# Kernel tuning notes

Hardware: AMD Instinct MI355X
Metric: run time of the kernel (lower is better)

The kernel has to match this reference:

```python
import jax, jax.numpy as jnp
import numpy as np

N, E = 50000, 800000
IN, HID, L, HEADS, OUT = 128, 256, 8, 8, 40
DH = HID // HEADS


def setup_inputs() -> dict:
    key = jax.random.key(0)
    ks = jax.random.split(key, 12)
    s = 0.05
    d = {}
    d["X"] = jax.random.normal(ks[0], (N, IN), jnp.float32)
    d["src"] = jax.random.randint(ks[1], (E,), 0, N, dtype=jnp.int32)
    d["dst"] = jax.random.randint(ks[2], (E,), 0, N, dtype=jnp.int32)
    d["Win"] = jax.random.normal(ks[3], (IN, HID), jnp.float32) * s
    d["bin_"] = jnp.zeros((HID,), jnp.float32)
    d["Wq"] = jax.random.normal(ks[4], (L, HID, HID), jnp.float32) * s
    d["Wk"] = jax.random.normal(ks[5], (L, HID, HID), jnp.float32) * s
    d["Wv"] = jax.random.normal(ks[6], (L, HID, HID), jnp.float32) * s
    d["bq"] = jnp.zeros((L, HID), jnp.float32)
    d["bk"] = jnp.zeros((L, HID), jnp.float32)
    d["bv"] = jnp.zeros((L, HID), jnp.float32)
    d["Wout"] = jax.random.normal(ks[7], (HID, OUT), jnp.float32) * s
    d["bout"] = jnp.zeros((OUT,), jnp.float32)
    return d


def _segment_softmax(e, seg, n):
    # e: [E, H] edge scores, seg: [E] destination node ids
    m = jax.ops.segment_max(e, seg, num_segments=n)
    ex = jnp.exp(e - m[seg])
    s = jax.ops.segment_sum(ex, seg, num_segments=n)
    return ex / s[seg]


def reference(X, src, dst, Win, bin_, Wq, Wk, Wv, bq, bk, bv, Wout, bout):
    n = X.shape[0]
    scaling = DH ** -0.5
    h = X @ Win + bin_  # in_proj: [N, HID]
    for l in range(L):  # fixed small layer stack
        q = (h @ Wq[l] + bq[l]).reshape(n, HEADS, DH) * scaling
        k = (h @ Wk[l] + bk[l]).reshape(n, HEADS, DH)
        v = (h @ Wv[l] + bv[l]).reshape(n, HEADS, DH)
        # SDDMM: per-edge, per-head dot product q[dst] . k[src]
        e = jnp.einsum('ehd,ehd->eh', q[dst], k[src])  # [E, HEADS]
        a = _segment_softmax(e, dst, n)                # softmax over in-edges of each dst
        # SpMM: weighted aggregation of source values into destinations
        h = jax.ops.segment_sum(a[..., None] * v[src], dst, num_segments=n).reshape(n, HID)
    return h @ Wout + bout  # predictor: [N, OUT]
```

## Files before the change

kernel.cpp:

```cpp
#include <hip/hip_runtime.h>
#include <hip/hip_bf16.h>
#include <hip/hip_fp16.h>

#define N_NODES 50000
#define MPAD    50048
#define N_EDGES 800000
#define IN_DIM  128
#define HID     256
#define QKVW    768
#define N_LAYERS 8
#define OUT_DIM 40
#define SCALING 0.17677669529663687f

typedef __attribute__((ext_vector_type(8))) _Float16 f16x8;
typedef __attribute__((ext_vector_type(4))) float f32x4;

__device__ __forceinline__ void gload_lds16(const void* g, void* l) {
    __builtin_amdgcn_global_load_lds(
        (__attribute__((address_space(1))) const unsigned int*)g,
        (__attribute__((address_space(3))) unsigned int*)l, 16, 0, 0);
}

__global__ void hist_kernel(const int* __restrict__ dst, int* __restrict__ cnt, int E) {
    int e = blockIdx.x * blockDim.x + threadIdx.x;
    if (e < E) atomicAdd(&cnt[dst[e]], 1);
}

__global__ __launch_bounds__(1024) void scan_kernel(const int* __restrict__ cnt,
                                                    int* __restrict__ row_off, int n) {
    __shared__ int buf[1024];
    __shared__ int carry_s;
    int tid = threadIdx.x;
    if (tid == 0) carry_s = 0;
    __syncthreads();
    for (int base = 0; base < n; base += 1024) {
        int i = base + tid;
        int x = (i < n) ? cnt[i] : 0;
        buf[tid] = x;
        __syncthreads();
        for (int off = 1; off < 1024; off <<= 1) {
            int y = (tid >= off) ? buf[tid - off] : 0;
            __syncthreads();
            buf[tid] += y;
            __syncthreads();
        }
        int carry = carry_s;
        if (i < n) row_off[i] = carry + buf[tid] - x;
        int total = buf[1023];
        __syncthreads();
        if (tid == 0) carry_s = carry + total;
        __syncthreads();
    }
    if (tid == 0) row_off[n] = carry_s;
}

__global__ void scatter_kernel(const int* __restrict__ src, const int* __restrict__ dst,
                               const int* __restrict__ row_off, int* __restrict__ cur,
                               int* __restrict__ csr_src, int E) {
    int e = blockIdx.x * blockDim.x + threadIdx.x;
    if (e < E) {
        int d = dst[e];
        int pos = row_off[d] + atomicAdd(&cur[d], 1);
        csr_src[pos] = src[e];
    }
}

__global__ void wqkv_cvt_kernel(const float* __restrict__ Wq, const float* __restrict__ Wk,
                                const float* __restrict__ Wv, _Float16* __restrict__ outw) {
    int i = blockIdx.x * blockDim.x + threadIdx.x;
    if (i >= N_LAYERS * QKVW * HID) return;
    int k = i & 255;
    int n = (i >> 8) % QKVW;
    int l = i / (QKVW * HID);
    int seg = n >> 8, nn = n & 255;
    const float* W = (seg == 0) ? Wq : (seg == 1) ? Wk : Wv;
    outw[i] = (_Float16)W[((size_t)l * HID + k) * HID + nn];
}

__global__ void win_cvt_kernel(const float* __restrict__ Win, _Float16* __restrict__ outw) {
    int i = blockIdx.x * blockDim.x + threadIdx.x;
    if (i >= HID * IN_DIM) return;
    int k = i & 127;
    int n = i >> 7;
    outw[i] = (_Float16)Win[(size_t)k * HID + n];
}

__global__ void wout_cvt_kernel(const float* __restrict__ Wout, _Float16* __restrict__ hi,
                                _Float16* __restrict__ lo) {
    int i = blockIdx.x * blockDim.x + threadIdx.x;
    if (i >= 128 * HID) return;
    int k = i & 255;
    int n = i >> 8;
    float v = (n < OUT_DIM) ? Wout[(size_t)k * OUT_DIM + n] : 0.f;
    _Float16 h = (_Float16)v;
    hi[i] = h;
    lo[i] = (_Float16)(v - (float)h);
}

__global__ void x_cvt_kernel(const float* __restrict__ X, _Float16* __restrict__ outx) {
    int i = blockIdx.x * blockDim.x + threadIdx.x;
    if (i >= MPAD * IN_DIM) return;
    int r = i >> 7;
    outx[i] = (_Float16)((r < N_NODES) ? X[i] : 0.f);
}

__global__ __launch_bounds__(256) void gemm16(
        const _Float16* __restrict__ A, const _Float16* __restrict__ B,
        const float* __restrict__ bias0, const float* __restrict__ bias1,
        const float* __restrict__ bias2, float scale0,
        _Float16* __restrict__ C, int K, int ldC) {
    __shared__ __align__(16) _Float16 lds[2 * 4096];
    _Float16* ldsA = lds;
    _Float16* ldsB = lds + 4096;

    const int tid  = threadIdx.x;
    const int lane = tid & 63;
    const int wave = tid >> 6;
    const int row0 = blockIdx.y * 128;
    const int n0   = blockIdx.x * 128;

    const int p0 = wave * 64 + lane;
    const int p1 = p0 + 256;
    auto srcoff = [&](int p, int grow0) -> size_t {
        int row = p >> 2, cir = p & 3;
        int sw  = (row & 3) ^ ((row >> 2) & 3);
        int sc  = cir ^ sw;
        return (size_t)(grow0 + row) * K + sc * 8;
    };
    const size_t offA0 = srcoff(p0, row0), offA1 = srcoff(p1, row0);
    const size_t offB0 = srcoff(p0, n0),   offB1 = srcoff(p1, n0);
    const int d0 = wave * 512;
    const int d1 = 2048 + wave * 512;

    const int mh = (wave >> 1) * 64;
    const int nh = (wave & 1) * 64;
    int aoff[4], boff[4];
#pragma unroll
    for (int f = 0; f < 4; ++f) {
        int ra = mh + f * 16 + (lane & 15);
        int ca = (lane >> 4) ^ ((ra & 3) ^ ((ra >> 2) & 3));
        aoff[f] = ra * 64 + ca * 16;
        int rb = nh + f * 16 + (lane & 15);
        int cb = (lane >> 4) ^ ((rb & 3) ^ ((rb >> 2) & 3));
        boff[f] = rb * 64 + cb * 16;
    }

    f32x4 acc[4][4];
#pragma unroll
    for (int i = 0; i < 4; ++i)
#pragma unroll
        for (int j = 0; j < 4; ++j) acc[i][j] = {0.f, 0.f, 0.f, 0.f};

    for (int k0 = 0; k0 < K; k0 += 32) {
        gload_lds16(A + offA0 + k0, ldsA + d0);
        gload_lds16(A + offA1 + k0, ldsA + d1);
        gload_lds16(B + offB0 + k0, ldsB + d0);
        gload_lds16(B + offB1 + k0, ldsB + d1);
        __syncthreads();
        f16x8 af[4];
#pragma unroll
        for (int i = 0; i < 4; ++i)
            af[i] = *reinterpret_cast<const f16x8*>(reinterpret_cast<const char*>(ldsA) + aoff[i]);
#pragma unroll
        for (int j = 0; j < 4; ++j) {
            f16x8 bf = *reinterpret_cast<const f16x8*>(reinterpret_cast<const char*>(ldsB) + boff[j]);
#pragma unroll
            for (int i = 0; i < 4; ++i)
                acc[i][j] = __builtin_amdgcn_mfma_f32_16x16x32_f16(af[i], bf, acc[i][j], 0, 0, 0);
        }
        __syncthreads();
    }

    const int seg = n0 >> 8;
    const float* bias = (seg == 0) ? bias0 : (seg == 1) ? bias1 : bias2;
    const float scale = (seg == 0) ? scale0 : 1.f;
    const int fq = lane >> 4;
    const int fr = lane & 15;
#pragma unroll
    for (int i = 0; i < 4; ++i) {
#pragma unroll
        for (int j = 0; j < 4; ++j) {
#pragma unroll
            for (int r = 0; r < 4; ++r) {
                int m = row0 + mh + i * 16 + fq * 4 + r;
                int n = n0 + nh + j * 16 + fr;
                float o = (acc[i][j][r] + bias[n & 255]) * scale;
                C[(size_t)m * ldC + n] = (_Float16)o;
            }
        }
    }
}

__global__ __launch_bounds__(256) void gemm_out(
        const _Float16* __restrict__ A, const _Float16* __restrict__ Bh,
        const _Float16* __restrict__ Bl, const float* __restrict__ bias,
        float* __restrict__ C, int K) {
    __shared__ __align__(16) _Float16 lds[3 * 4096];
    _Float16* ldsA  = lds;
    _Float16* ldsBh = lds + 4096;
    _Float16* ldsBl = lds + 8192;

    const int tid  = threadIdx.x;
    const int lane = tid & 63;
    const int wave = tid >> 6;
    const int row0 = blockIdx.y * 128;

    const int p0 = wave * 64 + lane;
    const int p1 = p0 + 256;
    auto srcoff = [&](int p, int grow0) -> size_t {
        int row = p >> 2, cir = p & 3;
        int sw  = (row & 3) ^ ((row >> 2) & 3);
        int sc  = cir ^ sw;
        return (size_t)(grow0 + row) * K + sc * 8;
    };
    const size_t offA0 = srcoff(p0, row0), offA1 = srcoff(p1, row0);
    const size_t offB0 = srcoff(p0, 0),    offB1 = srcoff(p1, 0);
    const int d0 = wave * 512;
    const int d1 = 2048 + wave * 512;

    const int mh = (wave >> 1) * 64;
    const int nh = (wave & 1) * 64;
    int aoff[4], boff[4];
#pragma unroll
    for (int f = 0; f < 4; ++f) {
        int ra = mh + f * 16 + (lane & 15);
        int ca = (lane >> 4) ^ ((ra & 3) ^ ((ra >> 2) & 3));
        aoff[f] = ra * 64 + ca * 16;
        int rb = nh + f * 16 + (lane & 15);
        int cb = (lane >> 4) ^ ((rb & 3) ^ ((rb >> 2) & 3));
        boff[f] = rb * 64 + cb * 16;
    }

    f32x4 acc[4][4];
#pragma unroll
    for (int i = 0; i < 4; ++i)
#pragma unroll
        for (int j = 0; j < 4; ++j) acc[i][j] = {0.f, 0.f, 0.f, 0.f};

    for (int k0 = 0; k0 < K; k0 += 32) {
        gload_lds16(A + offA0 + k0, ldsA + d0);
        gload_lds16(A + offA1 + k0, ldsA + d1);
        gload_lds16(Bh + offB0 + k0, ldsBh + d0);
        gload_lds16(Bh + offB1 + k0, ldsBh + d1);
        gload_lds16(Bl + offB0 + k0, ldsBl + d0);
        gload_lds16(Bl + offB1 + k0, ldsBl + d1);
        __syncthreads();
        f16x8 af[4];
#pragma unroll
        for (int i = 0; i < 4; ++i)
            af[i] = *reinterpret_cast<const f16x8*>(reinterpret_cast<const char*>(ldsA) + aoff[i]);
#pragma unroll
        for (int j = 0; j < 4; ++j) {
            f16x8 bh = *reinterpret_cast<const f16x8*>(reinterpret_cast<const char*>(ldsBh) + boff[j]);
            f16x8 bl = *reinterpret_cast<const f16x8*>(reinterpret_cast<const char*>(ldsBl) + boff[j]);
#pragma unroll
            for (int i = 0; i < 4; ++i) {
                acc[i][j] = __builtin_amdgcn_mfma_f32_16x16x32_f16(af[i], bh, acc[i][j], 0, 0, 0);
                acc[i][j] = __builtin_amdgcn_mfma_f32_16x16x32_f16(af[i], bl, acc[i][j], 0, 0, 0);
            }
        }
        __syncthreads();
    }

    const int fq = lane >> 4;
    const int fr = lane & 15;
#pragma unroll
    for (int i = 0; i < 4; ++i) {
#pragma unroll
        for (int j = 0; j < 4; ++j) {
#pragma unroll
            for (int r = 0; r < 4; ++r) {
                int m = row0 + mh + i * 16 + fq * 4 + r;
                int n = nh + j * 16 + fr;
                if (m < N_NODES && n < OUT_DIM)
                    C[(size_t)m * OUT_DIM + n] = acc[i][j][r] + bias[n];
            }
        }
    }
}

__global__ __launch_bounds__(256) void attn_kernel(
        const _Float16* __restrict__ qkv, const int* __restrict__ row_off,
        const int* __restrict__ csr_src, _Float16* __restrict__ h_out, int n) {
    int wave = threadIdx.x >> 6;
    int lane = threadIdx.x & 63;
    int node = blockIdx.x * 4 + wave;
    if (node >= n) return;
    const int loff = lane * 4;
    float4 qv;
    {
        float2 raw = *reinterpret_cast<const float2*>(&qkv[(size_t)node * QKVW + loff]);
        const __half2* h2 = reinterpret_cast<const __half2*>(&raw);
        float2 a = __half22float2(h2[0]), b = __half22float2(h2[1]);
        qv = make_float4(a.x, a.y, b.x, b.y);
    }
    float4 acc = make_float4(0.f, 0.f, 0.f, 0.f);
    float m = -INFINITY, s = 0.f;
    int beg = row_off[node], end = row_off[node + 1];
    int idx = beg;

#define LOAD_KV(slot, sn)                                                                 \
    float2 kr##slot, vr##slot;                                                            \
    {                                                                                     \
        const _Float16* base = qkv + (size_t)(sn) * QKVW;                                 \
        kr##slot = *reinterpret_cast<const float2*>(base + HID + loff);                   \
        vr##slot = *reinterpret_cast<const float2*>(base + 2 * HID + loff);               \
    }

#define DOT(slot, dvar)                                                                   \
    float dvar;                                                                           \
    {                                                                                     \
        const __half2* kh = reinterpret_cast<const __half2*>(&kr##slot);                  \
        float2 k01 = __half22float2(kh[0]), k23 = __half22float2(kh[1]);                  \
        dvar = qv.x * k01.x + qv.y * k01.y + qv.z * k23.x + qv.w * k23.y;                 \
        dvar += __shfl_xor(dvar, 1);                                                      \
        dvar += __shfl_xor(dvar, 2);                                                      \
        dvar += __shfl_xor(dvar, 4);                                                      \
    }

#define VADD(slot, p)                                                                     \
    {                                                                                     \
        const __half2* vh = reinterpret_cast<const __half2*>(&vr##slot);                  \
        float2 v01 = __half22float2(vh[0]), v23 = __half22float2(vh[1]);                  \
        acc.x = fmaf(p, v01.x, acc.x);                                                    \
        acc.y = fmaf(p, v01.y, acc.y);                                                    \
        acc.z = fmaf(p, v23.x, acc.z);                                                    \
        acc.w = fmaf(p, v23.y, acc.w);                                                    \
    }

    for (; idx + 3 < end; idx += 4) {
        int s0 = csr_src[idx], s1 = csr_src[idx + 1];
        int s2 = csr_src[idx + 2], s3 = csr_src[idx + 3];
        LOAD_KV(0, s0) LOAD_KV(1, s1) LOAD_KV(2, s2) LOAD_KV(3, s3)
        DOT(0, e0) DOT(1, e1) DOT(2, e2) DOT(3, e3)
        float mn = fmaxf(fmaxf(fmaxf(m, e0), fmaxf(e1, e2)), e3);
        float c  = __expf(m - mn);
        float p0 = __expf(e0 - mn), p1 = __expf(e1 - mn);
        float p2 = __expf(e2 - mn), p3 = __expf(e3 - mn);
        s = fmaf(s, c, (p0 + p1) + (p2 + p3));
        acc.x *= c; acc.y *= c; acc.z *= c; acc.w *= c;
        VADD(0, p0) VADD(1, p1) VADD(2, p2) VADD(3, p3)
        m = mn;
    }
    for (; idx < end; ++idx) {
        int s0 = csr_src[idx];
        LOAD_KV(0, s0)
        DOT(0, e0)
        float mn = fmaxf(m, e0);
        float c = __expf(m - mn);
        float p0 = __expf(e0 - mn);
        s = fmaf(s, c, p0);
        acc.x *= c; acc.y *= c; acc.z *= c; acc.w *= c;
        VADD(0, p0)
        m = mn;
    }
#undef LOAD_KV
#undef DOT
#undef VADD

    float inv = (s > 0.f) ? 1.f / s : 0.f;
    __half2 o01 = __floats2half2_rn(acc.x * inv, acc.y * inv);
    __half2 o23 = __floats2half2_rn(acc.z * inv, acc.w * inv);
    union { __half2 h2[2]; float2 f2; } u;
    u.h2[0] = o01; u.h2[1] = o23;
    *reinterpret_cast<float2*>(&h_out[(size_t)node * HID + loff]) = u.f2;
}

extern "C" void kernel_launch(void* const* d_in, const int* in_sizes, int n_in,
                              void* d_out, int out_size, void* d_ws, size_t ws_size,
                              hipStream_t stream) {
    const float* X    = (const float*)d_in[0];
    const int*   src  = (const int*)d_in[1];
    const int*   dst  = (const int*)d_in[2];
    const float* Win  = (const float*)d_in[3];
    const float* bin_ = (const float*)d_in[4];
    const float* Wq   = (const float*)d_in[5];
    const float* Wk   = (const float*)d_in[6];
    const float* Wv   = (const float*)d_in[7];
    const float* bq   = (const float*)d_in[8];
    const float* bk   = (const float*)d_in[9];
    const float* bv   = (const float*)d_in[10];
    const float* Wout = (const float*)d_in[11];
    const float* bout = (const float*)d_in[12];
    float* out = (float*)d_out;

    char* ws = (char*)d_ws;
    size_t off = 0;
    auto alloc = [&](size_t bytes) -> void* {
        void* p = ws + off;
        off = (off + bytes + 255) & ~(size_t)255;
        return p;
    };
    _Float16* qkv   = (_Float16*)alloc((size_t)MPAD * QKVW * 2);
    _Float16* h     = (_Float16*)alloc((size_t)MPAD * HID * 2);
    _Float16* Xf    = (_Float16*)alloc((size_t)MPAD * IN_DIM * 2);
    _Float16* Wqkvt = (_Float16*)alloc((size_t)N_LAYERS * QKVW * HID * 2);
    _Float16* Wint  = (_Float16*)alloc((size_t)HID * IN_DIM * 2);
    _Float16* Wot_h = (_Float16*)alloc((size_t)128 * HID * 2);
    _Float16* Wot_l = (_Float16*)alloc((size_t)128 * HID * 2);
    int* cnt     = (int*)alloc(sizeof(int) * N_NODES);
    int* row_off = (int*)alloc(sizeof(int) * (N_NODES + 1));
    int* csr_src = (int*)alloc(sizeof(int) * N_EDGES);

    hipMemsetAsync(cnt, 0, sizeof(int) * N_NODES, stream);
    hist_kernel<<<(N_EDGES + 255) / 256, 256, 0, stream>>>(dst, cnt, N_EDGES);
    scan_kernel<<<1, 1024, 0, stream>>>(cnt, row_off, N_NODES);
    hipMemsetAsync(cnt, 0, sizeof(int) * N_NODES, stream);
    scatter_kernel<<<(N_EDGES + 255) / 256, 256, 0, stream>>>(src, dst, row_off, cnt, csr_src, N_EDGES);

    {
        int t1 = N_LAYERS * QKVW * HID;
        wqkv_cvt_kernel<<<(t1 + 255) / 256, 256, 0, stream>>>(Wq, Wk, Wv, Wqkvt);
        int t2 = HID * IN_DIM;
        win_cvt_kernel<<<(t2 + 255) / 256, 256, 0, stream>>>(Win, Wint);
        int t3 = 128 * HID;
        wout_cvt_kernel<<<(t3 + 255) / 256, 256, 0, stream>>>(Wout, Wot_h, Wot_l);
        int t4 = MPAD * IN_DIM;
        x_cvt_kernel<<<(t4 + 255) / 256, 256, 0, stream>>>(X, Xf);
    }

    dim3 blk(256);
    gemm16<<<dim3(2, MPAD / 128), blk, 0, stream>>>(
        Xf, Wint, bin_, bin_, bin_, 1.f, h, IN_DIM, HID);

    for (int l = 0; l < N_LAYERS; ++l) {
        const _Float16* Bl = Wqkvt + (size_t)l * QKVW * HID;
        gemm16<<<dim3(6, MPAD / 128), blk, 0, stream>>>(
            h, Bl, bq + l * HID, bk + l * HID, bv + l * HID, SCALING, qkv, HID, QKVW);
        attn_kernel<<<(N_NODES + 3) / 4, blk, 0, stream>>>(
            qkv, row_off, csr_src, h, N_NODES);
    }
    gemm_out<<<dim3(1, MPAD / 128), blk, 0, stream>>>(
        h, Wot_h, Wot_l, bout, out, HID);
}
```

Measured before the change: 1.600 ms.

## Double-buffer GEMM LDS loads, template K loop, and use wave-shuffle scan

The GEMM kernels now prefetch the next K tile into a second LDS buffer while computing the current one. They use explicit vmcnt waits and raw barriers in place of load-then-sync. The K loop is templated and fully unrolled, and the grid is transposed so consecutive blocks walk rows of the same weight column tile. The one-block CSR scan now uses wave shuffles instead of a barrier-heavy LDS Hillis-Steele scan. LDS use doubles, and the hand-placed waitcnt counts depend on the exact load count per stage.

```diff
diff --git a/kernel.cpp b/kernel.cpp
--- a/kernel.cpp
+++ b/kernel.cpp
@@ -28,25 +28,37 @@
 
 __global__ __launch_bounds__(1024) void scan_kernel(const int* __restrict__ cnt,
                                                     int* __restrict__ row_off, int n) {
-    __shared__ int buf[1024];
+    __shared__ int wsum[16];
     __shared__ int carry_s;
     int tid = threadIdx.x;
+    int lane = tid & 63, wid = tid >> 6;
     if (tid == 0) carry_s = 0;
     __syncthreads();
     for (int base = 0; base < n; base += 1024) {
         int i = base + tid;
         int x = (i < n) ? cnt[i] : 0;
-        buf[tid] = x;
+        int v = x;
+#pragma unroll
+        for (int off = 1; off < 64; off <<= 1) {
+            int y = __shfl_up(v, off);
+            if (lane >= off) v += y;
+        }
+        if (lane == 63) wsum[wid] = v;
         __syncthreads();
-        for (int off = 1; off < 1024; off <<= 1) {
-            int y = (tid >= off) ? buf[tid - off] : 0;
-            __syncthreads();
-            buf[tid] += y;
-            __syncthreads();
-        }
+        if (wid == 0) {
+            int w = (lane < 16) ? wsum[lane] : 0;
+#pragma unroll
+            for (int off = 1; off < 16; off <<= 1) {
+                int y = __shfl_up(w, off);
+                if (lane >= off) w += y;
+            }
+            if (lane < 16) wsum[lane] = w;
+        }
+        __syncthreads();
+        int wbase = (wid > 0) ? wsum[wid - 1] : 0;
         int carry = carry_s;
-        if (i < n) row_off[i] = carry + buf[tid] - x;
-        int total = buf[1023];
+        if (i < n) row_off[i] = carry + wbase + v - x;
+        int total = wsum[15];
         __syncthreads();
         if (tid == 0) carry_s = carry + total;
         __syncthreads();
@@ -104,20 +116,20 @@
     outx[i] = (_Float16)((r < N_NODES) ? X[i] : 0.f);
 }
 
+template<int NT>
 __global__ __launch_bounds__(256) void gemm16(
         const _Float16* __restrict__ A, const _Float16* __restrict__ B,
         const float* __restrict__ bias0, const float* __restrict__ bias1,
         const float* __restrict__ bias2, float scale0,
-        _Float16* __restrict__ C, int K, int ldC) {
-    __shared__ __align__(16) _Float16 lds[2 * 4096];
-    _Float16* ldsA = lds;
-    _Float16* ldsB = lds + 4096;
+        _Float16* __restrict__ C, int ldC) {
+    __shared__ __align__(16) _Float16 lds[2][2 * 4096];
+    const int K = NT * 32;
 
     const int tid  = threadIdx.x;
     const int lane = tid & 63;
     const int wave = tid >> 6;
-    const int row0 = blockIdx.y * 128;
-    const int n0   = blockIdx.x * 128;
+    const int row0 = blockIdx.x * 128;
+    const int n0   = blockIdx.y * 128;
 
     const int p0 = wave * 64 + lane;
     const int p1 = p0 + 256;
@@ -151,24 +163,41 @@
 #pragma unroll
         for (int j = 0; j < 4; ++j) acc[i][j] = {0.f, 0.f, 0.f, 0.f};
 
-    for (int k0 = 0; k0 < K; k0 += 32) {
-        gload_lds16(A + offA0 + k0, ldsA + d0);
-        gload_lds16(A + offA1 + k0, ldsA + d1);
-        gload_lds16(B + offB0 + k0, ldsB + d0);
-        gload_lds16(B + offB1 + k0, ldsB + d1);
-        __syncthreads();
+    auto STAGE = [&](int b, int t) {
+        _Float16* LA = &lds[b][0];
+        _Float16* LB = &lds[b][4096];
+        const size_t k0 = (size_t)t * 32;
+        gload_lds16(A + offA0 + k0, LA + d0);
+        gload_lds16(A + offA1 + k0, LA + d1);
+        gload_lds16(B + offB0 + k0, LB + d0);
+        gload_lds16(B + offB1 + k0, LB + d1);
+    };
+
+    STAGE(0, 0);
+#pragma unroll
+    for (int t = 0; t < NT; ++t) {
+        const int cur = t & 1;
+        if (t + 1 < NT) {
+            STAGE(cur ^ 1, t + 1);
+            asm volatile("s_waitcnt vmcnt(4)" ::: "memory");
+        } else {
+            asm volatile("s_waitcnt vmcnt(0)" ::: "memory");
+        }
+        __builtin_amdgcn_s_barrier();
+        const char* baseA = (const char*)&lds[cur][0];
+        const char* baseB = (const char*)&lds[cur][4096];
         f16x8 af[4];
 #pragma unroll
         for (int i = 0; i < 4; ++i)
-            af[i] = *reinterpret_cast<const f16x8*>(reinterpret_cast<const char*>(ldsA) + aoff[i]);
+            af[i] = *reinterpret_cast<const f16x8*>(baseA + aoff[i]);
 #pragma unroll
         for (int j = 0; j < 4; ++j) {
-            f16x8 bf = *reinterpret_cast<const f16x8*>(reinterpret_cast<const char*>(ldsB) + boff[j]);
+            f16x8 bf = *reinterpret_cast<const f16x8*>(baseB + boff[j]);
 #pragma unroll
             for (int i = 0; i < 4; ++i)
                 acc[i][j] = __builtin_amdgcn_mfma_f32_16x16x32_f16(af[i], bf, acc[i][j], 0, 0, 0);
         }
-        __syncthreads();
+        __builtin_amdgcn_s_barrier();
     }
 
     const int seg = n0 >> 8;
@@ -195,15 +224,12 @@
         const _Float16* __restrict__ A, const _Float16* __restrict__ Bh,
         const _Float16* __restrict__ Bl, const float* __restrict__ bias,
         float* __restrict__ C, int K) {
-    __shared__ __align__(16) _Float16 lds[3 * 4096];
-    _Float16* ldsA  = lds;
-    _Float16* ldsBh = lds + 4096;
-    _Float16* ldsBl = lds + 8192;
+    __shared__ __align__(16) _Float16 lds[2][3 * 4096];
 
     const int tid  = threadIdx.x;
     const int lane = tid & 63;
     const int wave = tid >> 6;
-    const int row0 = blockIdx.y * 128;
+    const int row0 = blockIdx.x * 128;
 
     const int p0 = wave * 64 + lane;
     const int p1 = p0 + 256;
@@ -237,29 +263,48 @@
 #pragma unroll
         for (int j = 0; j < 4; ++j) acc[i][j] = {0.f, 0.f, 0.f, 0.f};
 
-    for (int k0 = 0; k0 < K; k0 += 32) {
-        gload_lds16(A + offA0 + k0, ldsA + d0);
-        gload_lds16(A + offA1 + k0, ldsA + d1);
-        gload_lds16(Bh + offB0 + k0, ldsBh + d0);
-        gload_lds16(Bh + offB1 + k0, ldsBh + d1);
-        gload_lds16(Bl + offB0 + k0, ldsBl + d0);
-        gload_lds16(Bl + offB1 + k0, ldsBl + d1);
-        __syncthreads();
+    auto STAGE = [&](int b, int t) {
+        _Float16* LA  = &lds[b][0];
+        _Float16* LBh = &lds[b][4096];
+        _Float16* LBl = &lds[b][8192];
+        const size_t k0 = (size_t)t * 32;
+        gload_lds16(A  + offA0 + k0, LA  + d0);
+        gload_lds16(A  + offA1 + k0, LA  + d1);
+        gload_lds16(Bh + offB0 + k0, LBh + d0);
+        gload_lds16(Bh + offB1 + k0, LBh + d1);
+        gload_lds16(Bl + offB0 + k0, LBl + d0);
+        gload_lds16(Bl + offB1 + k0, LBl + d1);
+    };
+
+    STAGE(0, 0);
+#pragma unroll
+    for (int t = 0; t < 8; ++t) {
+        const int cur = t & 1;
+        if (t + 1 < 8) {
+            STAGE(cur ^ 1, t + 1);
+            asm volatile("s_waitcnt vmcnt(6)" ::: "memory");
+        } else {
+            asm volatile("s_waitcnt vmcnt(0)" ::: "memory");
+        }
+        __builtin_amdgcn_s_barrier();
+        const char* baseA  = (const char*)&lds[cur][0];
+        const char* baseBh = (const char*)&lds[cur][4096];
+        const char* baseBl = (const char*)&lds[cur][8192];
         f16x8 af[4];
 #pragma unroll
         for (int i = 0; i < 4; ++i)
-            af[i] = *reinterpret_cast<const f16x8*>(reinterpret_cast<const char*>(ldsA) + aoff[i]);
+            af[i] = *reinterpret_cast<const f16x8*>(baseA + aoff[i]);
 #pragma unroll
         for (int j = 0; j < 4; ++j) {
-            f16x8 bh = *reinterpret_cast<const f16x8*>(reinterpret_cast<const char*>(ldsBh) + boff[j]);
-            f16x8 bl = *reinterpret_cast<const f16x8*>(reinterpret_cast<const char*>(ldsBl) + boff[j]);
+            f16x8 bh = *reinterpret_cast<const f16x8*>(baseBh + boff[j]);
+            f16x8 bl = *reinterpret_cast<const f16x8*>(baseBl + boff[j]);
 #pragma unroll
             for (int i = 0; i < 4; ++i) {
                 acc[i][j] = __builtin_amdgcn_mfma_f32_16x16x32_f16(af[i], bh, acc[i][j], 0, 0, 0);
                 acc[i][j] = __builtin_amdgcn_mfma_f32_16x16x32_f16(af[i], bl, acc[i][j], 0, 0, 0);
             }
         }
-        __syncthreads();
+        __builtin_amdgcn_s_barrier();
     }
 
     const int fq = lane >> 4;
@@ -420,16 +465,16 @@
     }
 
     dim3 blk(256);
-    gemm16<<<dim3(2, MPAD / 128), blk, 0, stream>>>(
-        Xf, Wint, bin_, bin_, bin_, 1.f, h, IN_DIM, HID);
+    gemm16<4><<<dim3(MPAD / 128, 2), blk, 0, stream>>>(
+        Xf, Wint, bin_, bin_, bin_, 1.f, h, HID);
 
     for (int l = 0; l < N_LAYERS; ++l) {
         const _Float16* Bl = Wqkvt + (size_t)l * QKVW * HID;
-        gemm16<<<dim3(6, MPAD / 128), blk, 0, stream>>>(
-            h, Bl, bq + l * HID, bk + l * HID, bv + l * HID, SCALING, qkv, HID, QKVW);
+        gemm16<8><<<dim3(MPAD / 128, 6), blk, 0, stream>>>(
+            h, Bl, bq + l * HID, bk + l * HID, bv + l * HID, SCALING, qkv, QKVW);
         attn_kernel<<<(N_NODES + 3) / 4, blk, 0, stream>>>(
             qkv, row_off, csr_src, h, N_NODES);
     }
-    gemm_out<<<dim3(1, MPAD / 128), blk, 0, stream>>>(
+    gemm_out<<<dim3(MPAD / 128, 1), blk, 0, stream>>>(
         h, Wot_h, Wot_l, bout, out, HID);
 }
```

Measured after the change: 1.518 ms. 5.1% less time.
